# Kernel tuning notes

Measured on AMD Instinct MI355X. Metric: run time of the kernel, lower is better.

The kernel has to match this reference:

```python
import jax, jax.numpy as jnp
import numpy as np

B, N, D, H = 8, 1024, 768, 12
HD = D // H  # head_dim = 64


def setup_inputs() -> dict:
    key = jax.random.key(0)
    ks = jax.random.split(key, 7)
    s = 1.0 / np.sqrt(D)  # xavier-ish scale for weights
    return {
        "x1": jax.random.normal(ks[0], (B, N, D), dtype=jnp.float32),
        "x2": jax.random.normal(ks[1], (B, N, D), dtype=jnp.float32),
        "Wq": jax.random.normal(ks[2], (D, D), dtype=jnp.float32) * s,
        "Wk": jax.random.normal(ks[3], (D, D), dtype=jnp.float32) * s,
        "Wv": jax.random.normal(ks[4], (D, D), dtype=jnp.float32) * s,
        "Wo": jax.random.normal(ks[5], (D, D), dtype=jnp.float32) * s,
        "bo": jnp.zeros((D,), dtype=jnp.float32),
    }


def _heads(x):
    # (B, N, D) -> (B, H, N, HD)
    return x.reshape(B, -1, H, HD).transpose(0, 2, 1, 3)


def reference(x1, x2, Wq, Wk, Wv, Wo, bo):
    scale = 1.0 / jnp.sqrt(jnp.asarray(HD, x1.dtype))
    q1 = _heads(x1 @ Wq.T)               # (B,H,N,HD)
    k1 = _heads(x1 @ Wk.T)
    v1 = _heads(x1 @ Wv.T)
    k2 = _heads(x2 @ Wk.T)
    v2 = _heads(x2 @ Wv.T)
    kc = jnp.concatenate([k1, k2], axis=2)   # (B,H,2N,HD)
    vc = jnp.concatenate([v1, v2], axis=2)
    attn = jnp.einsum('bhnd,bhmd->bhnm', q1, kc) * scale  # (B,H,N,2N)
    attn = jax.nn.softmax(attn, axis=-1)
    out = jnp.einsum('bhnm,bhmd->bhnd', attn, vc)          # (B,H,N,HD)
    out = out.transpose(0, 2, 1, 3).reshape(B, N, D)
    return out @ Wo.T + bo
```

## Files before the change

kernel.cpp:

```cpp
#include <hip/hip_runtime.h>


typedef __bf16 bf16x8 __attribute__((ext_vector_type(8)));
typedef float  f32x4  __attribute__((ext_vector_type(4)));
typedef unsigned int u32x4 __attribute__((ext_vector_type(4)));
typedef short  s16x4  __attribute__((ext_vector_type(4)));

__device__ __forceinline__ unsigned short bf16bits(float f) {
    return __builtin_bit_cast(unsigned short, (__bf16)f);
}
__device__ __forceinline__ unsigned pk2(float a, float b) {
    return (unsigned)bf16bits(a) | ((unsigned)bf16bits(b) << 16);
}
__device__ __forceinline__ bf16x8 asbf(u32x4 v) {
    return __builtin_bit_cast(bf16x8, v);
}
__device__ __forceinline__ float fexp2(float x) {
#if __has_builtin(__builtin_amdgcn_exp2f)
    return __builtin_amdgcn_exp2f(x);
#else
    return exp2f(x);
#endif
}
__device__ __forceinline__ float frcp(float x) {
#if __has_builtin(__builtin_amdgcn_rcpf)
    return __builtin_amdgcn_rcpf(x);
#else
    return 1.0f / x;
#endif
}

#if __has_builtin(__builtin_amdgcn_mfma_f32_16x16x16bf16_1k)
#define HAVE_MFMA16 1
#define MFMA16(a, b, c) __builtin_amdgcn_mfma_f32_16x16x16bf16_1k((a), (b), (c), 0, 0, 0)
#else
#define HAVE_MFMA16 0
#endif

__global__ __launch_bounds__(256) void convert_all(
    const float* __restrict__ x1, const float* __restrict__ x2,
    const float* __restrict__ Wq, const float* __restrict__ Wk,
    const float* __restrict__ Wv, const float* __restrict__ Wo,
    unsigned short* __restrict__ x1b, unsigned short* __restrict__ x2b,
    unsigned short* __restrict__ Wcat, unsigned short* __restrict__ Wob)
{
    const float* src; unsigned short* dst; int n4;
    switch (blockIdx.y) {
        case 0:  src = x1; dst = x1b;            n4 = 1572864; break;
        case 1:  src = x2; dst = x2b;            n4 = 1572864; break;
        case 2:  src = Wq; dst = Wcat;           n4 = 147456;  break;
        case 3:  src = Wk; dst = Wcat +  589824; n4 = 147456;  break;
        case 4:  src = Wv; dst = Wcat + 1179648; n4 = 147456;  break;
        default: src = Wo; dst = Wob;            n4 = 147456;  break;
    }
    int i = blockIdx.x * 256 + threadIdx.x;
    if (i >= n4) return;
    float4 v = ((const float4*)src)[i];
    unsigned* o32 = (unsigned*)(dst + (size_t)i * 4);
    o32[0] = pk2(v.x, v.y);
    o32[1] = pk2(v.z, v.w);
}

template<int MODE>
__global__ __launch_bounds__(256) void gemm_qkv(
    const unsigned short* __restrict__ A1, const unsigned short* __restrict__ A2,
    const unsigned short* __restrict__ Wcat,
    unsigned short* __restrict__ dQ, unsigned short* __restrict__ dK,
    unsigned short* __restrict__ dV, float* __restrict__ dO,
    const float* __restrict__ bias)
{
    __shared__ u32x4 smA[1024];
    __shared__ u32x4 smB[1024];

    const int tid  = threadIdx.x;
    const int lane = tid & 63;
    const int l15  = lane & 15;
    const int g    = lane >> 4;
    const int wid  = tid >> 6;
    const int rb   = blockIdx.x;
    const int jb   = blockIdx.y;
    const int wr   = (wid >> 1) * 64;
    const int wc   = (wid & 1) * 64;

    const bool br2 = (MODE == 0) && (jb >= 18);
    const unsigned short* A  = br2 ? A2 : A1;
    const unsigned short* Bw = br2 ? (Wcat + 589824) : Wcat;
    const int jcol = br2 ? (jb - 18) : jb;

    f32x4 acc[4][4] = {};

    for (int kt = 0; kt < 12; ++kt) {
        __syncthreads();
#pragma unroll
        for (int c_ = 0; c_ < 4; ++c_) {
            int i_   = (wid + c_ * 4) * 64 + lane;
            int row_ = i_ >> 3;
            int gs_  = (i_ & 7) ^ (row_ & 7);
            const unsigned short* sa = A +
                (size_t)(rb * 128 + row_) * 768 + kt * 64 + gs_ * 8;
            __builtin_amdgcn_global_load_lds(
                (const __attribute__((address_space(1))) void*)sa,
                (__attribute__((address_space(3))) void*)(smA + (wid + c_ * 4) * 64),
                16, 0, 0);
            const unsigned short* sb = Bw +
                (size_t)(jcol * 128 + row_) * 768 + kt * 64 + gs_ * 8;
            __builtin_amdgcn_global_load_lds(
                (const __attribute__((address_space(1))) void*)sb,
                (__attribute__((address_space(3))) void*)(smB + (wid + c_ * 4) * 64),
                16, 0, 0);
        }
        asm volatile("s_waitcnt vmcnt(0)" ::: "memory");
        __syncthreads();
        __builtin_amdgcn_sched_barrier(0);

#pragma unroll
        for (int kk = 0; kk < 2; ++kk) {
            bf16x8 af[4], bfr[4];
#pragma unroll
            for (int m = 0; m < 4; ++m) {
                int row = wr + m * 16 + l15;
                af[m] = asbf(smA[row * 8 + ((kk * 4 + g) ^ (row & 7))]);
            }
#pragma unroll
            for (int n = 0; n < 4; ++n) {
                int row = wc + n * 16 + l15;
                bfr[n] = asbf(smB[row * 8 + ((kk * 4 + g) ^ (row & 7))]);
            }
#pragma unroll
            for (int m = 0; m < 4; ++m)
#pragma unroll
                for (int n = 0; n < 4; ++n)
                    acc[m][n] = __builtin_amdgcn_mfma_f32_16x16x32_bf16(
                        af[m], bfr[n], acc[m][n], 0, 0, 0);
        }
    }

    const int rloc = wr + g * 4;
    const int cloc = wc + l15;
    const int seg  = jcol / 6;
#pragma unroll
    for (int m = 0; m < 4; ++m) {
#pragma unroll
        for (int n = 0; n < 4; ++n) {
            int r0 = rb * 128 + rloc + m * 16;
            int c  = jcol * 128 + cloc + n * 16;
            if constexpr (MODE == 2) {
#pragma unroll
                for (int reg = 0; reg < 4; ++reg)
                    dO[(size_t)(r0 + reg) * 768 + c] = acc[m][n][reg] + bias[c];
            } else {
                int b = r0 >> 10, nn = r0 & 1023;
                int cl = c - seg * 768;
                int h = cl >> 6, hd = cl & 63;
                int segq = br2 ? seg + 3 : seg;
                if (segq == 0) {
#pragma unroll
                    for (int reg = 0; reg < 4; ++reg)
                        dQ[((size_t)(b * 12 + h) * 1024 + nn + reg) * 64 + hd] =
                            bf16bits(acc[m][n][reg] * 0.18033688f);
                } else if (segq == 1 || segq == 3) {
                    size_t koff = (segq == 3) ? 1024 : 0;
#pragma unroll
                    for (int reg = 0; reg < 4; ++reg)
                        dK[((size_t)(b * 12 + h) * 2048 + koff + nn + reg) * 64 + hd] =
                            bf16bits(acc[m][n][reg]);
                } else {
                    size_t koff = (segq == 4) ? 1024 : 0;
                    uint2 w;
                    w.x = pk2(acc[m][n][0], acc[m][n][1]);
                    w.y = pk2(acc[m][n][2], acc[m][n][3]);
                    *(uint2*)(dV + ((size_t)(b * 12 + h) * 64 + hd) * 2048 + koff + nn) = w;
                }
            }
        }
    }
}

__global__ __launch_bounds__(256, 3) void attn_k(
    const unsigned short* __restrict__ Q, const unsigned short* __restrict__ K,
    const unsigned short* __restrict__ Vt, unsigned short* __restrict__ AO)
{
    __shared__ u32x4 sK[1024];
    __shared__ u32x4 sV[1024];
#if !HAVE_MFMA16
    __shared__ unsigned short sPT[8192];
#endif

    const int tid  = threadIdx.x;
    const int lane = tid & 63;
    const int g    = lane >> 4;
    const int l15  = lane & 15;
    const int wid  = tid >> 6;
    const int q0   = blockIdx.x * 128;
    const int bh   = blockIdx.y;

    const unsigned short* Qh = Q  + (size_t)bh * (1024 * 64);
    const unsigned short* Kh = K  + (size_t)bh * (2048 * 64);
    const unsigned short* Vh = Vt + (size_t)bh * (64 * 2048);

    bf16x8 qf[2][2];
#pragma unroll
    for (int m = 0; m < 2; ++m)
#pragma unroll
        for (int kk = 0; kk < 2; ++kk)
            qf[m][kk] = *(const bf16x8*)(Qh +
                (size_t)(q0 + wid * 32 + m * 16 + l15) * 64 + kk * 32 + g * 8);

    f32x4 o[4][2] = {};
    float lr0 = 0.f, lr1 = 0.f;

#define STAGE_TILE(T, DOFF)                                                          \
    {                                                                                \
        int t_ = (T);                                                                \
        _Pragma("unroll")                                                            \
        for (int c_ = 0; c_ < 2; ++c_) {                                             \
            int i_   = (wid + c_ * 4) * 64 + lane;                                   \
            int row_ = i_ >> 3;                                                      \
            int gs_  = (i_ & 7) ^ (row_ & 7);                                        \
            const unsigned short* srcK_ = Kh + ((size_t)t_ * 64 + row_) * 64 + gs_ * 8; \
            __builtin_amdgcn_global_load_lds(                                        \
                (const __attribute__((address_space(1))) void*)srcK_,               \
                (__attribute__((address_space(3))) void*)(sK + (DOFF) + (wid + c_ * 4) * 64), \
                16, 0, 0);                                                           \
            const unsigned short* srcV_ = Vh + (size_t)row_ * 2048 + t_ * 64 + gs_ * 8; \
            __builtin_amdgcn_global_load_lds(                                        \
                (const __attribute__((address_space(1))) void*)srcV_,               \
                (__attribute__((address_space(3))) void*)(sV + (DOFF) + (wid + c_ * 4) * 64), \
                16, 0, 0);                                                           \
        }                                                                            \
    }

    STAGE_TILE(0, 0)

    for (int t = 0; t < 32; ++t) {
        asm volatile("s_waitcnt vmcnt(0)" ::: "memory");
        __builtin_amdgcn_s_barrier();
        __builtin_amdgcn_sched_barrier(0);
        if (t < 31) STAGE_TILE(t + 1, (((t + 1) & 1) << 9))

        const u32x4* sKb = sK + ((t & 1) << 9);
        const u32x4* sVb = sV + ((t & 1) << 9);

        f32x4 s[4][2] = {};
        __builtin_amdgcn_s_setprio(1);
#pragma unroll
        for (int kk = 0; kk < 2; ++kk) {
            bf16x8 kf[4];
#pragma unroll
            for (int n = 0; n < 4; ++n) {
                int row = n * 16 + l15;
                kf[n] = asbf(sKb[row * 8 + ((kk * 4 + g) ^ (row & 7))]);
            }
#pragma unroll
            for (int n = 0; n < 4; ++n)
#pragma unroll
                for (int m = 0; m < 2; ++m)
                    s[n][m] = __builtin_amdgcn_mfma_f32_16x16x32_bf16(
                        kf[n], qf[m][kk], s[n][m], 0, 0, 0);
        }
        __builtin_amdgcn_s_setprio(0);

        float sum0 = 0.f, sum1 = 0.f;
#if HAVE_MFMA16
        s16x4 p16[4][2];
#pragma unroll
        for (int n = 0; n < 4; ++n) {
            float p00 = fexp2(s[n][0][0]), p01 = fexp2(s[n][0][1]);
            float p02 = fexp2(s[n][0][2]), p03 = fexp2(s[n][0][3]);
            float p10 = fexp2(s[n][1][0]), p11 = fexp2(s[n][1][1]);
            float p12 = fexp2(s[n][1][2]), p13 = fexp2(s[n][1][3]);
            sum0 += (p00 + p01) + (p02 + p03);
            sum1 += (p10 + p11) + (p12 + p13);
            p16[n][0] = (s16x4){ (short)bf16bits(p00), (short)bf16bits(p01),
                                 (short)bf16bits(p02), (short)bf16bits(p03) };
            p16[n][1] = (s16x4){ (short)bf16bits(p10), (short)bf16bits(p11),
                                 (short)bf16bits(p12), (short)bf16bits(p13) };
        }
        lr0 += sum0; lr1 += sum1;

        __builtin_amdgcn_s_setprio(1);
#pragma unroll
        for (int v = 0; v < 4; ++v) {
            int row = v * 16 + l15;
            const unsigned short* vrow = (const unsigned short*)sVb + row * 64;
#pragma unroll
            for (int n = 0; n < 4; ++n) {
                int gpos = (2 * n + (g >> 1)) ^ (row & 7);
                s16x4 vv = *(const s16x4*)(vrow + gpos * 8 + (g & 1) * 4);
#pragma unroll
                for (int m = 0; m < 2; ++m)
                    o[v][m] = MFMA16(vv, p16[n][m], o[v][m]);
            }
        }
        __builtin_amdgcn_s_setprio(0);
#else
#pragma unroll
        for (int n = 0; n < 4; ++n)
#pragma unroll
            for (int r = 0; r < 4; ++r) {
                float p0 = fexp2(s[n][0][r]);
                float p1 = fexp2(s[n][1][r]);
                s[n][0][r] = p0; s[n][1][r] = p1;
                sum0 += p0; sum1 += p1;
            }
        lr0 += sum0; lr1 += sum1;
#pragma unroll
        for (int m = 0; m < 2; ++m) {
            int row = wid * 32 + m * 16 + l15;
            int sw  = (row & 7) << 1;
#pragma unroll
            for (int n = 0; n < 4; ++n) {
                uint2 w;
                w.x = pk2(s[n][m][0], s[n][m][1]);
                w.y = pk2(s[n][m][2], s[n][m][3]);
                *(uint2*)(sPT + row * 64 + (((n * 4 + g) ^ sw) << 2)) = w;
            }
        }
        __builtin_amdgcn_s_setprio(1);
#pragma unroll
        for (int c = 0; c < 2; ++c) {
            bf16x8 pf[2], vf[4];
#pragma unroll
            for (int m = 0; m < 2; ++m) {
                int row = wid * 32 + m * 16 + l15;
                pf[m] = *(const bf16x8*)(sPT + row * 64 + (((4 * c + g) ^ (row & 7)) << 3));
            }
#pragma unroll
            for (int v = 0; v < 4; ++v) {
                int row = v * 16 + l15;
                vf[v] = asbf(sVb[row * 8 + ((4 * c + g) ^ (row & 7))]);
            }
#pragma unroll
            for (int v = 0; v < 4; ++v)
#pragma unroll
                for (int m = 0; m < 2; ++m)
                    o[v][m] = __builtin_amdgcn_mfma_f32_16x16x32_bf16(
                        vf[v], pf[m], o[v][m], 0, 0, 0);
        }
        __builtin_amdgcn_s_setprio(0);
#endif
    }

    lr0 += __shfl_xor(lr0, 16); lr0 += __shfl_xor(lr0, 32);
    lr1 += __shfl_xor(lr1, 16); lr1 += __shfl_xor(lr1, 32);
    const int b = bh / 12, h = bh % 12;
    float rl0 = frcp(lr0), rl1 = frcp(lr1);
#pragma unroll
    for (int m = 0; m < 2; ++m) {
        float rl = m ? rl1 : rl0;
        int q = q0 + wid * 32 + m * 16 + l15;
        unsigned short* dst = AO + (size_t)(b * 1024 + q) * 768 + h * 64 + g * 4;
#pragma unroll
        for (int v = 0; v < 4; ++v) {
            uint2 w;
            w.x = pk2(o[v][m][0] * rl, o[v][m][1] * rl);
            w.y = pk2(o[v][m][2] * rl, o[v][m][3] * rl);
            *(uint2*)(dst + v * 16) = w;
        }
    }
#undef STAGE_TILE
}

extern "C" void kernel_launch(void* const* d_in, const int* in_sizes, int n_in,
                              void* d_out, int out_size, void* d_ws, size_t ws_size,
                              hipStream_t stream)
{
    const float* x1 = (const float*)d_in[0];
    const float* x2 = (const float*)d_in[1];
    const float* Wq = (const float*)d_in[2];
    const float* Wk = (const float*)d_in[3];
    const float* Wv = (const float*)d_in[4];
    const float* Wo = (const float*)d_in[5];
    const float* bo = (const float*)d_in[6];

    unsigned short* Wcat = (unsigned short*)d_ws;
    unsigned short* Wob  = Wcat + 1769472;
    unsigned short* x1b  = Wob  + 589824;
    unsigned short* x2b  = x1b  + 6291456;
    unsigned short* Qb   = x2b  + 6291456;
    unsigned short* Kc   = Qb   + 6291456;
    unsigned short* Vt   = Kc   + 12582912;
    unsigned short* AO   = x1b;

    convert_all<<<dim3(6144, 6), 256, 0, stream>>>(x1, x2, Wq, Wk, Wv, Wo,
                                                   x1b, x2b, Wcat, Wob);

    gemm_qkv<0><<<dim3(64, 30), 256, 0, stream>>>(x1b, x2b, Wcat,
                                                  Qb, Kc, Vt, nullptr, nullptr);

    attn_k<<<dim3(8, 96), 256, 0, stream>>>(Qb, Kc, Vt, AO);

    gemm_qkv<2><<<dim3(64, 6), 256, 0, stream>>>(AO, nullptr, Wob,
                                                 nullptr, nullptr, nullptr,
                                                 (float*)d_out, bo);
}
```

Before: 175.6 us.

## Triple-buffer K/V tiles, permute V layout for 128-bit LDS reads, swap grid order

The attention kernel's K/V staging goes from double to triple buffering. Loads run two tiles ahead and wait with vmcnt(4) instead of draining all outstanding loads each iteration. The QKV GEMM epilogue now writes V with a permutation inside each 64-column tile, so the PV step can read one 128-bit LDS vector per lane and split it into two 16x16x16 MFMA operands instead of doing two 64-bit reads. The grid is transposed so consecutive blocks share the same query tile across heads, and the fallback path without MFMA16 is removed. The larger shared-memory footprint may lower occupancy relative to the launch_bounds target of 3 blocks.

```diff
diff --git a/kernel.cpp b/kernel.cpp
--- a/kernel.cpp
+++ b/kernel.cpp
@@ -5,6 +5,7 @@
 typedef float  f32x4  __attribute__((ext_vector_type(4)));
 typedef unsigned int u32x4 __attribute__((ext_vector_type(4)));
 typedef short  s16x4  __attribute__((ext_vector_type(4)));
+typedef short  s16x8  __attribute__((ext_vector_type(8)));
 
 __device__ __forceinline__ unsigned short bf16bits(float f) {
     return __builtin_bit_cast(unsigned short, (__bf16)f);
@@ -30,12 +31,7 @@
 #endif
 }
 
-#if __has_builtin(__builtin_amdgcn_mfma_f32_16x16x16bf16_1k)
-#define HAVE_MFMA16 1
 #define MFMA16(a, b, c) __builtin_amdgcn_mfma_f32_16x16x16bf16_1k((a), (b), (c), 0, 0, 0)
-#else
-#define HAVE_MFMA16 0
-#endif
 
 __global__ __launch_bounds__(256) void convert_all(
     const float* __restrict__ x1, const float* __restrict__ x2,
@@ -166,10 +162,14 @@
                             bf16bits(acc[m][n][reg]);
                 } else {
                     size_t koff = (segq == 4) ? 1024 : 0;
+                    int kv = (int)koff + nn;
+                    int tt = kv >> 6, u = kv & 63;
+                    int up = ((u & 12) << 2) | ((u & 48) >> 2) | (u & 3);
                     uint2 w;
                     w.x = pk2(acc[m][n][0], acc[m][n][1]);
                     w.y = pk2(acc[m][n][2], acc[m][n][3]);
-                    *(uint2*)(dV + ((size_t)(b * 12 + h) * 64 + hd) * 2048 + koff + nn) = w;
+                    *(uint2*)(dV + ((size_t)(b * 12 + h) * 64 + hd) * 2048 +
+                              tt * 64 + up) = w;
                 }
             }
         }
@@ -180,19 +180,16 @@
     const unsigned short* __restrict__ Q, const unsigned short* __restrict__ K,
     const unsigned short* __restrict__ Vt, unsigned short* __restrict__ AO)
 {
-    __shared__ u32x4 sK[1024];
-    __shared__ u32x4 sV[1024];
-#if !HAVE_MFMA16
-    __shared__ unsigned short sPT[8192];
-#endif
+    __shared__ u32x4 sK[1536];
+    __shared__ u32x4 sV[1536];
 
     const int tid  = threadIdx.x;
     const int lane = tid & 63;
     const int g    = lane >> 4;
     const int l15  = lane & 15;
     const int wid  = tid >> 6;
-    const int q0   = blockIdx.x * 128;
-    const int bh   = blockIdx.y;
+    const int bh   = blockIdx.x;
+    const int q0   = blockIdx.y * 128;
 
     const unsigned short* Qh = Q  + (size_t)bh * (1024 * 64);
     const unsigned short* Kh = K  + (size_t)bh * (2048 * 64);
@@ -231,15 +228,19 @@
     }
 
     STAGE_TILE(0, 0)
+    STAGE_TILE(1, 512)
 
     for (int t = 0; t < 32; ++t) {
-        asm volatile("s_waitcnt vmcnt(0)" ::: "memory");
+        if (t < 31) { asm volatile("s_waitcnt vmcnt(4)" ::: "memory"); }
+        else        { asm volatile("s_waitcnt vmcnt(0)" ::: "memory"); }
         __builtin_amdgcn_s_barrier();
+        if (t < 30) {
+            STAGE_TILE(t + 2, ((t + 2) % 3) * 512)
+        }
         __builtin_amdgcn_sched_barrier(0);
-        if (t < 31) STAGE_TILE(t + 1, (((t + 1) & 1) << 9))
-
-        const u32x4* sKb = sK + ((t & 1) << 9);
-        const u32x4* sVb = sV + ((t & 1) << 9);
+
+        const u32x4* sKb = sK + (t % 3) * 512;
+        const u32x4* sVb = sV + (t % 3) * 512;
 
         f32x4 s[4][2] = {};
         __builtin_amdgcn_s_setprio(1);
@@ -261,7 +262,6 @@
         __builtin_amdgcn_s_setprio(0);
 
         float sum0 = 0.f, sum1 = 0.f;
-#if HAVE_MFMA16
         s16x4 p16[4][2];
 #pragma unroll
         for (int n = 0; n < 4; ++n) {
@@ -282,63 +282,22 @@
 #pragma unroll
         for (int v = 0; v < 4; ++v) {
             int row = v * 16 + l15;
-            const unsigned short* vrow = (const unsigned short*)sVb + row * 64;
-#pragma unroll
-            for (int n = 0; n < 4; ++n) {
-                int gpos = (2 * n + (g >> 1)) ^ (row & 7);
-                s16x4 vv = *(const s16x4*)(vrow + gpos * 8 + (g & 1) * 4);
+            int rho = row & 7;
+#pragma unroll
+            for (int hb = 0; hb < 2; ++hb) {
+                s16x8 vv = __builtin_bit_cast(s16x8,
+                    sVb[row * 8 + ((2 * g + hb) ^ rho)]);
+                s16x4 lo = __builtin_shufflevector(vv, vv, 0, 1, 2, 3);
+                s16x4 hi = __builtin_shufflevector(vv, vv, 4, 5, 6, 7);
 #pragma unroll
                 for (int m = 0; m < 2; ++m)
-                    o[v][m] = MFMA16(vv, p16[n][m], o[v][m]);
+                    o[v][m] = MFMA16(lo, p16[2 * hb][m], o[v][m]);
+#pragma unroll
+                for (int m = 0; m < 2; ++m)
+                    o[v][m] = MFMA16(hi, p16[2 * hb + 1][m], o[v][m]);
             }
         }
         __builtin_amdgcn_s_setprio(0);
-#else
-#pragma unroll
-        for (int n = 0; n < 4; ++n)
-#pragma unroll
-            for (int r = 0; r < 4; ++r) {
-                float p0 = fexp2(s[n][0][r]);
-                float p1 = fexp2(s[n][1][r]);
-                s[n][0][r] = p0; s[n][1][r] = p1;
-                sum0 += p0; sum1 += p1;
-            }
-        lr0 += sum0; lr1 += sum1;
-#pragma unroll
-        for (int m = 0; m < 2; ++m) {
-            int row = wid * 32 + m * 16 + l15;
-            int sw  = (row & 7) << 1;
-#pragma unroll
-            for (int n = 0; n < 4; ++n) {
-                uint2 w;
-                w.x = pk2(s[n][m][0], s[n][m][1]);
-                w.y = pk2(s[n][m][2], s[n][m][3]);
-                *(uint2*)(sPT + row * 64 + (((n * 4 + g) ^ sw) << 2)) = w;
-            }
-        }
-        __builtin_amdgcn_s_setprio(1);
-#pragma unroll
-        for (int c = 0; c < 2; ++c) {
-            bf16x8 pf[2], vf[4];
-#pragma unroll
-            for (int m = 0; m < 2; ++m) {
-                int row = wid * 32 + m * 16 + l15;
-                pf[m] = *(const bf16x8*)(sPT + row * 64 + (((4 * c + g) ^ (row & 7)) << 3));
-            }
-#pragma unroll
-            for (int v = 0; v < 4; ++v) {
-                int row = v * 16 + l15;
-                vf[v] = asbf(sVb[row * 8 + ((4 * c + g) ^ (row & 7))]);
-            }
-#pragma unroll
-            for (int v = 0; v < 4; ++v)
-#pragma unroll
-                for (int m = 0; m < 2; ++m)
-                    o[v][m] = __builtin_amdgcn_mfma_f32_16x16x32_bf16(
-                        vf[v], pf[m], o[v][m], 0, 0, 0);
-        }
-        __builtin_amdgcn_s_setprio(0);
-#endif
     }
 
     lr0 += __shfl_xor(lr0, 16); lr0 += __shfl_xor(lr0, 32);
@@ -388,7 +347,7 @@
     gemm_qkv<0><<<dim3(64, 30), 256, 0, stream>>>(x1b, x2b, Wcat,
                                                   Qb, Kc, Vt, nullptr, nullptr);
 
-    attn_k<<<dim3(8, 96), 256, 0, stream>>>(Qb, Kc, Vt, AO);
+    attn_k<<<dim3(96, 8), 256, 0, stream>>>(Qb, Kc, Vt, AO);
 
     gemm_qkv<2><<<dim3(64, 6), 256, 0, stream>>>(AO, nullptr, Wob,
                                                  nullptr, nullptr, nullptr,
```

Result: no change. 174.1 us (-0.9%).
